# Kernel optimization log

Measured on AMD Instinct MI355X. Metric: run time of the kernel, lower is better.

Reference implementation:

```python
import jax, jax.numpy as jnp
import numpy as np

THR = 0.2          # config['thr']
BORDER_RM = 2      # config['border_rm']
TEMP = 0.1         # config['dsmax_temperature']


def setup_inputs() -> dict:
    key = jax.random.key(0)
    k0, k1 = jax.random.split(key)
    N, C = 2, 256
    h0c, w0c, h1c, w1c = 60, 80, 60, 80
    return {
        "feat_c0": jax.random.normal(k0, (N, h0c * w0c, C), dtype=jnp.float32),
        "feat_c1": jax.random.normal(k1, (N, h1c * w1c, C), dtype=jnp.float32),
        "h0c": h0c, "w0c": w0c, "h1c": h1c, "w1c": w1c,
    }


def _valid_1d(n: int, b: int):
    # True in the interior [b, n-b), False on the border — matches mask_border writes
    return jnp.zeros((n,), dtype=bool).at[b:n - b].set(True)


def reference(feat_c0, feat_c1, h0c, w0c, h1c, w1c):
    N, L, C = feat_c0.shape
    S = feat_c1.shape[1]
    scale = 1.0 / (C ** 0.5)
    f0 = feat_c0 * scale
    f1 = feat_c1 * scale

    # similarity + dual softmax  -> conf_matrix [N, L, S]
    sim = jnp.einsum('nlc,nsc->nls', f0, f1) / TEMP
    conf = jax.nn.softmax(sim, axis=1) * jax.nn.softmax(sim, axis=2)

    # threshold + border removal (mask_border, vectorized as an interior mask)
    mask = conf > THR
    b = BORDER_RM
    border = (_valid_1d(h0c, b)[:, None, None, None]
              & _valid_1d(w0c, b)[None, :, None, None]
              & _valid_1d(h1c, b)[None, None, :, None]
              & _valid_1d(w1c, b)[None, None, None, :])  # [h0c,w0c,h1c,w1c]
    mask = (mask.reshape(N, h0c, w0c, h1c, w1c) & border[None]).reshape(N, L, S)

    # mutual nearest neighbor
    mask = mask \
        & (conf == conf.max(axis=2, keepdims=True)) \
        & (conf == conf.max(axis=1, keepdims=True))

    # match extraction, expressed densely (static shapes for jit):
    # mask_v[b,i] = row i of pair b has a match; j_ids its column; mconf its confidence
    mask_v = mask.any(axis=2)                               # [N, L]
    j_ids = jnp.argmax(mask, axis=2)                        # [N, L] (first True)
    mconf = jnp.take_along_axis(conf, j_ids[:, :, None], axis=2)[..., 0]
    mconf = jnp.where(mask_v, mconf, 0.0)                   # [N, L]

    # coarse keypoint coords for matched columns: (x, y) = (j % w1c, j // w1c)
    mkpts1_c = jnp.stack([j_ids % w1c, j_ids // w1c], axis=-1)  # [N, L, 2]

    return conf, mask_v, j_ids, mkpts1_c, mconf
```

## Files before the change

kernel.cpp:

```cpp
#include <hip/hip_runtime.h>

typedef _Float16 half8 __attribute__((ext_vector_type(8)));
typedef float f32x4 __attribute__((ext_vector_type(4)));

#define NB 2
#define LS 4800
#define CCH 256
#define W0 80
#define W1 80
#define THRV 0.2f
#define SQS 0.19764235376052370f

#define TN 38
#define PADL 4864
#define NWG (TN * TN * NB)
#define CPX (NWG / 8)

#define OF_RST  0
#define OF_CST  19200
#define OF_RWM  38400
#define OF_CAND 48000
#define OF_CLM  57600
#define OF_PROW 67200
#define OF_PCOL (67200 + 739328)
#define OF_AH   (67200 + 2*739328)
#define OF_BH   (OF_AH + 1228800)

#define O_MASKV 46080000ull
#define O_JIDS  46089600ull
#define O_MKPT  46099200ull
#define O_MCONF 46118400ull

__device__ __forceinline__ void load_lds16(const void* g, void* l) {
    __builtin_amdgcn_global_load_lds((const __attribute__((address_space(1))) void*)g,
                                     (__attribute__((address_space(3))) void*)l, 16, 0, 0);
}

__device__ __forceinline__ void swizzle_ids(int& n, int& by, int& bx) {
    const int orig = ((int)blockIdx.z * TN + (int)blockIdx.y) * TN + (int)blockIdx.x;
    const int wg = (orig & 7) * CPX + (orig >> 3);
    n = wg / (TN * TN);
    const int rem = wg % (TN * TN);
    by = rem / TN; bx = rem % TN;
}

__global__ __launch_bounds__(256) void conv_half(const float* __restrict__ A,
                                                 const float* __restrict__ B,
                                                 float* __restrict__ ws) {
    const int which = blockIdx.y;
    const float* src = which ? B : A;
    _Float16* dst = (_Float16*)(ws + (which ? OF_BH : OF_AH));
    const int idx = blockIdx.x * 256 + threadIdx.x;
    const float4 v = ((const float4*)src)[idx];
    union { _Float16 h[4]; uint2 u; } p;
    p.h[0] = (_Float16)(v.x * SQS);
    p.h[1] = (_Float16)(v.y * SQS);
    p.h[2] = (_Float16)(v.z * SQS);
    p.h[3] = (_Float16)(v.w * SQS);
    ((uint2*)dst)[idx] = p.u;
}

__device__ __forceinline__ void gemm_core(const _Float16* __restrict__ Ah,
                                          const _Float16* __restrict__ Bh,
                                          _Float16* smA, _Float16* smB,
                                          const int bx, const int by,
                                          const int tid, f32x4 (&acc)[4][4]) {
    const int lane = tid & 63, w = tid >> 6;
    const int wx = w & 1, wy = w >> 1;
    const int m = lane & 15, quad = lane >> 4;
    const int srow = lane >> 3;
    const int qst = (lane & 7) ^ (srow & 7);

    for (int kt = 0; kt < 4; kt++) {
        const int k0 = kt * 64;
#pragma unroll
        for (int i = 0; i < 4; i++) {
            const int c = i * 4 + w;
            int gr = by * 128 + c * 8 + srow; gr = gr < LS ? gr : LS - 1;
            load_lds16(Ah + (size_t)gr * CCH + k0 + qst * 8, &smA[c * 512]);
        }
#pragma unroll
        for (int i = 0; i < 4; i++) {
            const int c = i * 4 + w;
            int gr = bx * 128 + c * 8 + srow; gr = gr < LS ? gr : LS - 1;
            load_lds16(Bh + (size_t)gr * CCH + k0 + qst * 8, &smB[c * 512]);
        }
        __syncthreads();
#pragma unroll
        for (int t = 0; t < 2; t++) {
            half8 Af[4], Bf[4];
#pragma unroll
            for (int a = 0; a < 4; a++) {
                const int rl = wy * 64 + a * 16 + m;
                const int sl = rl * 8 + ((t * 4 + quad) ^ (rl & 7));
                Af[a] = *(const half8*)&smA[sl * 8];
            }
#pragma unroll
            for (int b = 0; b < 4; b++) {
                const int cl = wx * 64 + b * 16 + m;
                const int sl = cl * 8 + ((t * 4 + quad) ^ (cl & 7));
                Bf[b] = *(const half8*)&smB[sl * 8];
            }
#pragma unroll
            for (int a = 0; a < 4; a++)
#pragma unroll
                for (int b = 0; b < 4; b++)
                    acc[a][b] = __builtin_amdgcn_mfma_f32_16x16x32_f16(Af[a], Bf[b], acc[a][b], 0, 0, 0);
        }
        __syncthreads();
    }
}

__global__ __launch_bounds__(256, 3) void gemm_stats(float* __restrict__ ws) {
    __shared__ __align__(16) union {
        struct { _Float16 A[8192]; _Float16 B[8192]; } st;
        struct { float rs[128][2][2]; float cs[128][2][2]; } red;
    } sm;
    int n, by, bx;
    swizzle_ids(n, by, bx);
    const _Float16* Ah = (const _Float16*)(ws + OF_AH) + (size_t)n * LS * CCH;
    const _Float16* Bh = (const _Float16*)(ws + OF_BH) + (size_t)n * LS * CCH;
    const int tid = threadIdx.x;
    const int lane = tid & 63, w = tid >> 6;
    const int wx = w & 1, wy = w >> 1;
    const int m = lane & 15, quad = lane >> 4;

    f32x4 acc[4][4];
    {
        f32x4 z = {0.f, 0.f, 0.f, 0.f};
#pragma unroll
        for (int a = 0; a < 4; a++)
#pragma unroll
            for (int b = 0; b < 4; b++) acc[a][b] = z;
    }
    gemm_core(Ah, Bh, sm.st.A, sm.st.B, bx, by, tid, acc);

    const int l0 = by * 128, s0 = bx * 128;
    bool bval[4];
#pragma unroll
    for (int b = 0; b < 4; b++) bval[b] = (s0 + wx * 64 + b * 16 + m) < LS;

    float T = -1e30f;
#pragma unroll
    for (int a = 0; a < 4; a++)
#pragma unroll
        for (int reg = 0; reg < 4; reg++) {
            if ((l0 + wy * 64 + a * 16 + quad * 4 + reg) < LS) {
#pragma unroll
                for (int b = 0; b < 4; b++)
                    if (bval[b]) T = fmaxf(T, acc[a][b][reg]);
            }
        }
#pragma unroll
    for (int d = 1; d < 64; d <<= 1) T = fmaxf(T, __shfl_xor(T, d, 64));

#pragma unroll
    for (int a = 0; a < 4; a++)
#pragma unroll
        for (int reg = 0; reg < 4; reg++) {
            const bool rv = (l0 + wy * 64 + a * 16 + quad * 4 + reg) < LS;
#pragma unroll
            for (int b = 0; b < 4; b++)
                acc[a][b][reg] = (rv && bval[b]) ? __expf(acc[a][b][reg] - T) : 0.f;
        }

#pragma unroll
    for (int a = 0; a < 4; a++)
#pragma unroll
        for (int reg = 0; reg < 4; reg++) {
            float s = acc[a][0][reg] + acc[a][1][reg] + acc[a][2][reg] + acc[a][3][reg];
#pragma unroll
            for (int d = 1; d < 16; d <<= 1) s += __shfl_xor(s, d, 64);
            if (m == 0) {
                const int rl = wy * 64 + a * 16 + quad * 4 + reg;
                sm.red.rs[rl][wx][0] = T; sm.red.rs[rl][wx][1] = s;
            }
        }
#pragma unroll
    for (int b = 0; b < 4; b++) {
        float s = 0.f;
#pragma unroll
        for (int a = 0; a < 4; a++)
#pragma unroll
            for (int reg = 0; reg < 4; reg++) s += acc[a][b][reg];
        s += __shfl_xor(s, 16, 64);
        s += __shfl_xor(s, 32, 64);
        if (quad == 0) {
            const int cl = wx * 64 + b * 16 + m;
            sm.red.cs[cl][wy][0] = T; sm.red.cs[cl][wy][1] = s;
        }
    }
    __syncthreads();
    if (tid < 128) {
        const float m0 = sm.red.rs[tid][0][0], v0 = sm.red.rs[tid][0][1];
        const float m1 = sm.red.rs[tid][1][0], v1 = sm.red.rs[tid][1][1];
        const float nm = fmaxf(m0, m1);
        const float s = v0 * __expf(m0 - nm) + v1 * __expf(m1 - nm);
        ((float2*)(ws + OF_PROW))[((size_t)n * PADL + by * 128 + tid) * TN + bx] = make_float2(nm, s);
    } else {
        const int t = tid - 128;
        const float m0 = sm.red.cs[t][0][0], v0 = sm.red.cs[t][0][1];
        const float m1 = sm.red.cs[t][1][0], v1 = sm.red.cs[t][1][1];
        const float nm = fmaxf(m0, m1);
        const float s = v0 * __expf(m0 - nm) + v1 * __expf(m1 - nm);
        ((float2*)(ws + OF_PCOL))[((size_t)n * PADL + bx * 128 + t) * TN + by] = make_float2(nm, s);
    }
}

__global__ __launch_bounds__(256) void combine_stats(float* __restrict__ ws) {
    const int idx = blockIdx.x * 256 + threadIdx.x;
    const int half_ = idx >= 9600;
    const int i = idx - half_ * 9600;
    const int n = i / LS, r = i % LS;
    const float2* P = (const float2*)(ws + (half_ ? OF_PCOL : OF_PROW)) + ((size_t)n * PADL + r) * TN;
    float M = -1e30f, S = 0.f;
    for (int b = 0; b < TN; b++) {
        const float2 p = P[b];
        const float nm = fmaxf(M, p.x);
        S = S * __expf(M - nm) + p.y * __expf(p.x - nm);
        M = nm;
    }
    ((float2*)(ws + (half_ ? OF_CST : OF_RST)))[n * LS + r] = make_float2(M, 1.0f / S);
}

__global__ __launch_bounds__(256, 3) void gemm_conf(float* __restrict__ out,
                                                    float* __restrict__ ws) {
    __shared__ __align__(16) union {
        struct { _Float16 A[8192]; _Float16 B[8192]; } st;
        struct { float rst[128][2]; float cst[128][2];
                 float rsv[128][2][2]; float csv[128][2]; } ep;
    } sm;
    int n, by, bx;
    swizzle_ids(n, by, bx);
    const _Float16* Ah = (const _Float16*)(ws + OF_AH) + (size_t)n * LS * CCH;
    const _Float16* Bh = (const _Float16*)(ws + OF_BH) + (size_t)n * LS * CCH;
    const int tid = threadIdx.x;
    const int lane = tid & 63, w = tid >> 6;
    const int wx = w & 1, wy = w >> 1;
    const int m = lane & 15, quad = lane >> 4;

    f32x4 acc[4][4];
    {
        f32x4 z = {0.f, 0.f, 0.f, 0.f};
#pragma unroll
        for (int a = 0; a < 4; a++)
#pragma unroll
            for (int b = 0; b < 4; b++) acc[a][b] = z;
    }
    gemm_core(Ah, Bh, sm.st.A, sm.st.B, bx, by, tid, acc);

    const int l0 = by * 128, s0 = bx * 128;
    if (tid < 128) {
        int r = l0 + tid; r = r < LS ? r : LS - 1;
        const float2 v = ((const float2*)(ws + OF_RST))[n * LS + r];
        sm.ep.rst[tid][0] = v.x; sm.ep.rst[tid][1] = v.y;
    } else {
        const int t = tid - 128;
        int c = s0 + t; c = c < LS ? c : LS - 1;
        const float2 v = ((const float2*)(ws + OF_CST))[n * LS + c];
        sm.ep.cst[t][0] = v.x; sm.ep.cst[t][1] = v.y;
    }
    __syncthreads();

    float* On = out + (size_t)n * LS * LS;
    float colm[4] = {-1.f, -1.f, -1.f, -1.f};
    bool bval[4]; int gc4[4]; float cmx[4], csi[4];
#pragma unroll
    for (int b = 0; b < 4; b++) {
        const int cl = wx * 64 + b * 16 + m;
        gc4[b] = s0 + cl;
        bval[b] = gc4[b] < LS;
        cmx[b] = sm.ep.cst[cl][0]; csi[b] = sm.ep.cst[cl][1];
    }
#pragma unroll
    for (int a = 0; a < 4; a++) {
#pragma unroll
        for (int reg = 0; reg < 4; reg++) {
            const int rl = wy * 64 + a * 16 + quad * 4 + reg;
            const int gr = l0 + rl;
            const float rm = sm.ep.rst[rl][0], rsi = sm.ep.rst[rl][1];
            const bool rv = gr < LS;
            float bestv = -1.f; int besti = 0;
#pragma unroll
            for (int b = 0; b < 4; b++) {
                const float c = __expf(2.f * acc[a][b][reg] - rm - cmx[b]) * (rsi * csi[b]);
                if (rv && bval[b]) {
                    On[(size_t)gr * LS + gc4[b]] = c;
                    if (c > bestv) { bestv = c; besti = gc4[b]; }
                    colm[b] = fmaxf(colm[b], c);
                }
            }
#pragma unroll
            for (int d = 1; d < 16; d <<= 1) {
                const float ov = __shfl_xor(bestv, d, 64);
                const int oi = __shfl_xor(besti, d, 64);
                if (ov > bestv || (ov == bestv && oi < besti)) { bestv = ov; besti = oi; }
            }
            if (m == 0) {
                sm.ep.rsv[rl][wx][0] = bestv;
                sm.ep.rsv[rl][wx][1] = __int_as_float(besti);
            }
        }
    }
#pragma unroll
    for (int b = 0; b < 4; b++) {
        float v = colm[b];
        v = fmaxf(v, __shfl_xor(v, 16, 64));
        v = fmaxf(v, __shfl_xor(v, 32, 64));
        if (quad == 0) sm.ep.csv[wx * 64 + b * 16 + m][wy] = v;
    }
    __syncthreads();
    if (tid < 128) {
        const float v0 = sm.ep.rsv[tid][0][0]; const int i0 = __float_as_int(sm.ep.rsv[tid][0][1]);
        const float v1 = sm.ep.rsv[tid][1][0]; const int i1 = __float_as_int(sm.ep.rsv[tid][1][1]);
        float bv; int bi;
        if (v0 > v1 || (v0 == v1 && i0 <= i1)) { bv = v0; bi = i0; } else { bv = v1; bi = i1; }
        ((float2*)(ws + OF_PROW))[((size_t)n * PADL + by * 128 + tid) * TN + bx] =
            make_float2(bv, __int_as_float(bi));
    } else {
        const int t = tid - 128;
        const float v = fmaxf(sm.ep.csv[t][0], sm.ep.csv[t][1]);
        (ws + OF_PCOL)[((size_t)n * PADL + bx * 128 + t) * TN + by] = v;
    }
}

__global__ __launch_bounds__(256) void combine_max(float* __restrict__ ws) {
    const int idx = blockIdx.x * 256 + threadIdx.x;
    const int half_ = idx >= 9600;
    const int i = idx - half_ * 9600;
    const int n = i / LS, r = i % LS;
    if (!half_) {
        const float2* P = (const float2*)(ws + OF_PROW) + ((size_t)n * PADL + r) * TN;
        float bv = -2.f; int bi = 0;
        for (int b = 0; b < TN; b++) {
            const float2 p = P[b];
            const int pi = __float_as_int(p.y);
            if (p.x > bv || (p.x == bv && pi < bi)) { bv = p.x; bi = pi; }
        }
        ws[OF_RWM + i] = bv;
        ((int*)ws)[OF_CAND + i] = bi;
    } else {
        const float* P = ws + OF_PCOL + ((size_t)n * PADL + r) * TN;
        float v = -2.f;
        for (int b = 0; b < TN; b++) v = fmaxf(v, P[b]);
        ws[OF_CLM + i] = v;
    }
}

__global__ __launch_bounds__(256) void match_pass(const float* __restrict__ ws,
                                                  float* __restrict__ out) {
    const int idx = blockIdx.x * 256 + threadIdx.x;
    if (idx >= NB * LS) return;
    const int n = idx / LS, l = idx % LS;
    const float rwm = ws[OF_RWM + idx];
    const int cand = ((const int*)ws)[OF_CAND + idx];
    const float clm = ws[OF_CLM + n * LS + cand];
    const int y0 = l / W0, x0 = l % W0;
    const int y1 = cand / W1, x1 = cand % W1;
    const bool b0 = (y0 >= 2 && y0 < 58 && x0 >= 2 && x0 < 78);
    const bool b1 = (y1 >= 2 && y1 < 58 && x1 >= 2 && x1 < 78);
    const bool matched = (rwm > THRV) && b0 && b1 && (rwm == clm);
    const int j = matched ? cand : 0;
    out[O_MASKV + idx] = matched ? 1.f : 0.f;
    out[O_JIDS + idx] = (float)j;
    out[O_MKPT + (size_t)idx * 2 + 0] = (float)(j % W1);
    out[O_MKPT + (size_t)idx * 2 + 1] = (float)(j / W1);
    out[O_MCONF + idx] = matched ? rwm : 0.f;
}

extern "C" void kernel_launch(void* const* d_in, const int* in_sizes, int n_in,
                              void* d_out, int out_size, void* d_ws, size_t ws_size,
                              hipStream_t stream) {
    const float* f0 = (const float*)d_in[0];
    const float* f1 = (const float*)d_in[1];
    float* out = (float*)d_out;
    float* ws = (float*)d_ws;

    conv_half<<<dim3(2400, 2), 256, 0, stream>>>(f0, f1, ws);
    gemm_stats<<<dim3(TN, TN, NB), 256, 0, stream>>>(ws);
    combine_stats<<<75, 256, 0, stream>>>(ws);
    gemm_conf<<<dim3(TN, TN, NB), 256, 0, stream>>>(out, ws);
    combine_max<<<75, 256, 0, stream>>>(ws);
    match_pass<<<38, 256, 0, stream>>>(ws, out);
}
```

Measured before the change: 307.5 us.

## Double-buffer LDS tiles in GEMM core with K-step of 32

Restructures the GEMM inner loop so the K dimension is processed in 8 steps of 32 instead of 4 steps of 64. The LDS tiles are split into two 4096-element buffers, and the next step's global-to-LDS loads are issued before the current step's MFMAs. The intent is to overlap memory latency with compute and to cut the barriers per step from two to one. The swizzle changes to match the 4-chunk row layout, and the shorter K-step means less work per barrier and more loop iterations.

```diff
diff --git a/kernel.cpp b/kernel.cpp
--- a/kernel.cpp
+++ b/kernel.cpp
@@ -68,47 +68,60 @@
     const int lane = tid & 63, w = tid >> 6;
     const int wx = w & 1, wy = w >> 1;
     const int m = lane & 15, quad = lane >> 4;
-    const int srow = lane >> 3;
-    const int qst = (lane & 7) ^ (srow & 7);
-
-    for (int kt = 0; kt < 4; kt++) {
-        const int k0 = kt * 64;
-#pragma unroll
-        for (int i = 0; i < 4; i++) {
-            const int c = i * 4 + w;
-            int gr = by * 128 + c * 8 + srow; gr = gr < LS ? gr : LS - 1;
-            load_lds16(Ah + (size_t)gr * CCH + k0 + qst * 8, &smA[c * 512]);
-        }
-#pragma unroll
-        for (int i = 0; i < 4; i++) {
-            const int c = i * 4 + w;
-            int gr = bx * 128 + c * 8 + srow; gr = gr < LS ? gr : LS - 1;
-            load_lds16(Bh + (size_t)gr * CCH + k0 + qst * 8, &smB[c * 512]);
-        }
+    const int rr = lane >> 2;
+    const int q = (lane & 3) ^ ((lane >> 3) & 3);
+
+    const _Float16* ga[2];
+    const _Float16* gb[2];
+#pragma unroll
+    for (int i = 0; i < 2; i++) {
+        const int c = w * 2 + i;
+        int gra = by * 128 + c * 16 + rr; gra = gra < LS ? gra : LS - 1;
+        int grb = bx * 128 + c * 16 + rr; grb = grb < LS ? grb : LS - 1;
+        ga[i] = Ah + (size_t)gra * CCH + q * 8;
+        gb[i] = Bh + (size_t)grb * CCH + q * 8;
+    }
+
+#pragma unroll
+    for (int i = 0; i < 2; i++) {
+        const int c = w * 2 + i;
+        load_lds16(ga[i], &smA[c * 512]);
+        load_lds16(gb[i], &smB[c * 512]);
+    }
+
+    for (int kt = 0; kt < 8; kt++) {
         __syncthreads();
-#pragma unroll
-        for (int t = 0; t < 2; t++) {
-            half8 Af[4], Bf[4];
-#pragma unroll
-            for (int a = 0; a < 4; a++) {
-                const int rl = wy * 64 + a * 16 + m;
-                const int sl = rl * 8 + ((t * 4 + quad) ^ (rl & 7));
-                Af[a] = *(const half8*)&smA[sl * 8];
-            }
-#pragma unroll
-            for (int b = 0; b < 4; b++) {
-                const int cl = wx * 64 + b * 16 + m;
-                const int sl = cl * 8 + ((t * 4 + quad) ^ (cl & 7));
-                Bf[b] = *(const half8*)&smB[sl * 8];
-            }
-#pragma unroll
-            for (int a = 0; a < 4; a++)
-#pragma unroll
-                for (int b = 0; b < 4; b++)
-                    acc[a][b] = __builtin_amdgcn_mfma_f32_16x16x32_f16(Af[a], Bf[b], acc[a][b], 0, 0, 0);
-        }
-        __syncthreads();
-    }
+        const int cur = (kt & 1) * 4096;
+        if (kt < 7) {
+            const int nxt = 4096 - cur;
+            const int ko = (kt + 1) * 32;
+#pragma unroll
+            for (int i = 0; i < 2; i++) {
+                const int c = w * 2 + i;
+                load_lds16(ga[i] + ko, &smA[nxt + c * 512]);
+                load_lds16(gb[i] + ko, &smB[nxt + c * 512]);
+            }
+        }
+        half8 Af[4], Bf[4];
+#pragma unroll
+        for (int a = 0; a < 4; a++) {
+            const int rl = wy * 64 + a * 16 + m;
+            const int sl = rl * 4 + (quad ^ ((rl >> 1) & 3));
+            Af[a] = *(const half8*)&smA[cur + sl * 8];
+        }
+#pragma unroll
+        for (int b = 0; b < 4; b++) {
+            const int cl = wx * 64 + b * 16 + m;
+            const int sl = cl * 4 + (quad ^ ((cl >> 1) & 3));
+            Bf[b] = *(const half8*)&smB[cur + sl * 8];
+        }
+#pragma unroll
+        for (int a = 0; a < 4; a++)
+#pragma unroll
+            for (int b = 0; b < 4; b++)
+                acc[a][b] = __builtin_amdgcn_mfma_f32_16x16x32_f16(Af[a], Bf[b], acc[a][b], 0, 0, 0);
+    }
+    __syncthreads();
 }
 
 __global__ __launch_bounds__(256, 3) void gemm_stats(float* __restrict__ ws) {
```

Result: no change. 306.4 us (-0.4%).
